# Performance work log

Measured on AMD Instinct MI355X. Metric: run time of the kernel, lower is better.

## Reference

```python
import jax, jax.numpy as jnp
import numpy as np
import math


def setup_inputs() -> dict:
    key = jax.random.key(0)
    kq, kk, kv = jax.random.split(key, 3)
    B, H, N, d = 4, 16, 4096, 128
    return {
        "query": jax.random.normal(kq, (B, H, N, d), dtype=jnp.float32),
        "key": jax.random.normal(kk, (B, H, N, d), dtype=jnp.float32),
        "value": jax.random.normal(kv, (B, H, N, d), dtype=jnp.float32),
        "Br": 128,
        "Bc": 128,
    }


def reference(query, key, value, Br, Bc):
    """Tiled FlashAttention with online softmax (non-MX path of the module).

    Math per inner-loop iteration j (matches _inner_loop_body_sequential):
      scores = Q @ K_j^T * (1/sqrt(d))       (accumulate_fp32=True -> fp32)
      m_new  = max(m, scores.max(-1))
      alpha  = exp(m - m_new)
      P      = exp(scores - m_new)
      l      = alpha*l + P.sum(-1)
      O      = alpha*O + P @ V_j
    Final: out = O / l
    """
    B, H, N, d = query.shape
    Tc = N // Bc
    sm_scale = jnp.float32(1.0 / math.sqrt(d))

    # KV tiles: [Tc, B, H, Bc, d]
    k_tiles = jnp.moveaxis(key.reshape(B, H, Tc, Bc, d), 2, 0)
    v_tiles = jnp.moveaxis(value.reshape(B, H, Tc, Bc, d), 2, 0)

    q = query.astype(jnp.float32)

    O0 = jnp.zeros((B, H, N, d), dtype=jnp.float32)
    l0 = jnp.zeros((B, H, N, 1), dtype=jnp.float32)
    m0 = jnp.full((B, H, N, 1), -jnp.inf, dtype=jnp.float32)

    def body(carry, kv):
        O_i, l_i, m_i = carry
        Kj, Vj = kv  # [B, H, Bc, d]
        s = jnp.einsum("bhqd,bhkd->bhqk", q, Kj.astype(jnp.float32)) * sm_scale
        m_new = jnp.maximum(m_i, jnp.max(s, axis=-1, keepdims=True))
        alpha = jnp.exp(m_i - m_new)
        P = jnp.exp(s - m_new)
        l_new = alpha * l_i + jnp.sum(P, axis=-1, keepdims=True)
        O_new = alpha * O_i + jnp.einsum("bhqk,bhkd->bhqd", P, Vj.astype(jnp.float32))
        return (O_new, l_new, m_new), None

    (O_f, l_f, _), _ = jax.lax.scan(body, (O0, l0, m0), (k_tiles, v_tiles))
    out = O_f / l_f
    return out.astype(query.dtype)
```

## Files before the change

### kernel.cpp

```cpp
#include <hip/hip_runtime.h>
#include <math.h>


#define DHEAD 128
#define SEQ 4096
#define BR 128
#define BC 64
#define TC (SEQ / BC)
#define KSTR 136
#define VSTR 72

#define AS1 __attribute__((address_space(1)))
#define AS3 __attribute__((address_space(3)))

typedef __attribute__((ext_vector_type(8))) short short8;
typedef __attribute__((ext_vector_type(4))) float floatx4;
typedef __attribute__((ext_vector_type(2))) float floatx2;
typedef __attribute__((ext_vector_type(16))) float floatx16;

union U8 { unsigned u[4]; short8 s; };

__device__ __forceinline__ unsigned pk(float a, float b) {
    unsigned ua = __float_as_uint(a) + 0x8000u;
    unsigned ub = __float_as_uint(b) + 0x8000u;
    return __builtin_amdgcn_perm(ub, ua, 0x07060302);
}

__global__ __launch_bounds__(256) void conv_kv(const float* __restrict__ K,
                                               const float* __restrict__ V,
                                               short* __restrict__ Kb,
                                               short* __restrict__ Vb) {
    __shared__ float vt[64 * 133];
    const int blk = blockIdx.x;
    const float* Kh = K + (size_t)blk * (BC * DHEAD);
    const float* Vh = V + (size_t)blk * (BC * DHEAD);
    short* kb = Kb + (size_t)blk * (BC * DHEAD);
    short* vb = Vb + (size_t)blk * (BC * DHEAD);
    const int t = threadIdx.x;

#pragma unroll
    for (int i = 0; i < 4; ++i) {
        int c = i * 256 + t;
        int row = c >> 4;
        int d0 = (((c & 15) ^ ((row & 7) << 1)) << 3);
        const float* s = Kh + row * DHEAD + d0;
        floatx4 f0 = *(const floatx4*)s;
        floatx4 f1 = *(const floatx4*)(s + 4);
        U8 u;
        u.u[0] = pk(f0[0], f0[1]);
        u.u[1] = pk(f0[2], f0[3]);
        u.u[2] = pk(f1[0], f1[1]);
        u.u[3] = pk(f1[2], f1[3]);
        *(short8*)(kb + c * 8) = u.s;
    }

    {
        int n = t >> 2;
        int c0 = (t & 3) * 32;
        const float* s = Vh + n * DHEAD + c0;
        float* d = vt + n * 133 + c0;
#pragma unroll
        for (int j = 0; j < 8; ++j) *(floatx4*)(d + j * 4) = *(const floatx4*)(s + j * 4);
    }
    __syncthreads();

#pragma unroll
    for (int i = 0; i < 4; ++i) {
        int c = i * 256 + t;
        int row = c >> 3;
        int n0 = (((c & 7) ^ (row & 7)) << 3);
        float f[8];
#pragma unroll
        for (int j = 0; j < 8; ++j) f[j] = vt[(n0 + j) * 133 + row];
        U8 u;
        u.u[0] = pk(f[0], f[1]);
        u.u[1] = pk(f[2], f[3]);
        u.u[2] = pk(f[4], f[5]);
        u.u[3] = pk(f[6], f[7]);
        *(short8*)(vb + c * 8) = u.s;
    }
}

__launch_bounds__(256, 3)
__global__ void fa_fwd_ws(const float* __restrict__ Q, const short* __restrict__ Kb,
                          const short* __restrict__ Vb, float* __restrict__ Out) {
    __shared__ __attribute__((aligned(16))) short K_lds[BC * DHEAD];
    __shared__ __attribute__((aligned(16))) short VT_lds[DHEAD * BC];

    int x = blockIdx.x;
    int xcd = x & 7;
    int g = x >> 3;
    int q_tile = g & 31;
    int head = ((g >> 5) << 3) + xcd;

    const float* Qh = Q + (size_t)head * SEQ * DHEAD;
    const short* kbh = Kb + (size_t)head * (SEQ * DHEAD);
    const short* vbh = Vb + (size_t)head * (SEQ * DHEAD);
    float* Oh = Out + (size_t)head * SEQ * DHEAD;

    const int tid = threadIdx.x;
    const int wave = tid >> 6;
    const int lane = tid & 63;
    const int lm = lane & 31;
    const int h = lane >> 5;

    const int q0 = q_tile * BR;
    const int qw = wave * 32;

    const int kx = (lm & 7) << 4;
    const int vx = (lm & 7) << 3;

    const float cscale = 0.12751743f;
    short8 bq[8];
    {
        const float* qrow = Qh + (size_t)(q0 + qw + lm) * DHEAD;
#pragma unroll
        for (int s = 0; s < 8; ++s) {
            floatx4 f0 = *(const floatx4*)(qrow + s * 16 + h * 8);
            floatx4 f1 = *(const floatx4*)(qrow + s * 16 + h * 8 + 4);
            U8 t;
            t.u[0] = pk(f0[0] * cscale, f0[1] * cscale);
            t.u[1] = pk(f0[2] * cscale, f0[3] * cscale);
            t.u[2] = pk(f1[0] * cscale, f1[1] * cscale);
            t.u[3] = pk(f1[2] * cscale, f1[3] * cscale);
            bq[s] = t.s;
        }
    }

    floatx16 oacc[4];
#pragma unroll
    for (int i = 0; i < 4; ++i) oacc[i] = (floatx16)0.0f;
    float l_acc = 0.0f;

    for (int kt = 0; kt < TC; ++kt) {
        __syncthreads();

        {
            const short* kg = kbh + kt * 8192 + wave * 2048 + lane * 8;
            const short* vg = vbh + kt * 8192 + wave * 2048 + lane * 8;
            short* kl = (short*)K_lds + wave * 2048;
            short* vl = (short*)VT_lds + wave * 2048;
#pragma unroll
            for (int i = 0; i < 4; ++i) {
                __builtin_amdgcn_global_load_lds((const AS1 unsigned int*)(kg + i * 512),
                                                 (AS3 unsigned int*)(kl + i * 512), 16, 0, 0);
                __builtin_amdgcn_global_load_lds((const AS1 unsigned int*)(vg + i * 512),
                                                 (AS3 unsigned int*)(vl + i * 512), 16, 0, 0);
            }
        }
        __syncthreads();

        floatx16 sacc[2];
        sacc[0] = (floatx16)0.0f;
        sacc[1] = (floatx16)0.0f;
        __builtin_amdgcn_s_setprio(1);
#pragma unroll
        for (int kc = 0; kc < 8; ++kc) {
#pragma unroll
            for (int nt = 0; nt < 2; ++nt) {
                short8 a = *(const short8*)&K_lds[(nt * 32 + lm) * 128 + ((kc * 16 + h * 8) ^ kx)];
                sacc[nt] = __builtin_amdgcn_mfma_f32_32x32x16_bf16(a, bq[kc], sacc[nt], 0, 0, 0);
            }
        }
        __builtin_amdgcn_s_setprio(0);

#pragma unroll
        for (int nt = 0; nt < 2; ++nt) {
            float e[16];
#pragma unroll
            for (int r = 0; r < 16; ++r) e[r] = exp2f(sacc[nt][r]);
            float t8[8];
#pragma unroll
            for (int i = 0; i < 8; ++i) t8[i] = e[i] + e[8 + i];
            float t4[4];
#pragma unroll
            for (int i = 0; i < 4; ++i) t4[i] = t8[i] + t8[4 + i];
            l_acc += (t4[0] + t4[1]) + (t4[2] + t4[3]);

#pragma unroll
            for (int hf = 0; hf < 2; ++hf) {
                const int b0 = hf * 8;
                unsigned u0 = pk(e[b0 + 0], e[b0 + 1]);
                unsigned u1 = pk(e[b0 + 2], e[b0 + 3]);
                unsigned u2 = pk(e[b0 + 4], e[b0 + 5]);
                unsigned u3 = pk(e[b0 + 6], e[b0 + 7]);
                auto s1 = __builtin_amdgcn_permlane32_swap(u0, u2, false, false);
                auto s2 = __builtin_amdgcn_permlane32_swap(u1, u3, false, false);
                U8 t;
                t.u[0] = s1[0];
                t.u[1] = s2[0];
                t.u[2] = s1[1];
                t.u[3] = s2[1];
                const int kc2 = nt * 2 + hf;
                __builtin_amdgcn_s_setprio(1);
#pragma unroll
                for (int dt = 0; dt < 4; ++dt) {
                    short8 b = *(const short8*)&VT_lds[(dt * 32 + lm) * 64 + ((kc2 * 16 + h * 8) ^ vx)];
                    oacc[dt] = __builtin_amdgcn_mfma_f32_32x32x16_bf16(t.s, b, oacc[dt], 0, 0, 0);
                }
                __builtin_amdgcn_s_setprio(0);
            }
        }
    }

    float l_full = l_acc + __shfl_xor(l_acc, 32);
    float rl[16];
#pragma unroll
    for (int r = 0; r < 16; ++r) {
        int qr = (r & 3) + 8 * (r >> 2) + 4 * h;
        rl[r] = 1.0f / __shfl(l_full, qr);
    }
#pragma unroll
    for (int dt = 0; dt < 4; ++dt)
#pragma unroll
        for (int r = 0; r < 16; ++r) {
            int qr = (r & 3) + 8 * (r >> 2) + 4 * h;
            Oh[(size_t)(q0 + qw + qr) * DHEAD + dt * 32 + lm] = oacc[dt][r] * rl[r];
        }
}

__launch_bounds__(256, 3)
__global__ void fa_fwd(const float* __restrict__ Q, const float* __restrict__ K,
                       const float* __restrict__ V, float* __restrict__ Out) {
    __shared__ __attribute__((aligned(16))) short K_lds[BC * KSTR];
    __shared__ __attribute__((aligned(16))) short VT_lds[DHEAD * VSTR];

    int x = blockIdx.x;
    int xcd = x & 7;
    int g = x >> 3;
    int q_tile = g & 31;
    int head = ((g >> 5) << 3) + xcd;

    const float* Qh = Q + (size_t)head * SEQ * DHEAD;
    const float* Kh = K + (size_t)head * SEQ * DHEAD;
    const float* Vh = V + (size_t)head * SEQ * DHEAD;
    float* Oh = Out + (size_t)head * SEQ * DHEAD;

    const int tid = threadIdx.x;
    const int wave = tid >> 6;
    const int lane = tid & 63;
    const int lm = lane & 31;
    const int h = lane >> 5;

    const int q0 = q_tile * BR;
    const int qw = wave * 32;

    const float cscale = 0.12751743f;
    short8 bq[8];
    {
        const float* qrow = Qh + (size_t)(q0 + qw + lm) * DHEAD;
#pragma unroll
        for (int s = 0; s < 8; ++s) {
            floatx4 f0 = *(const floatx4*)(qrow + s * 16 + h * 8);
            floatx4 f1 = *(const floatx4*)(qrow + s * 16 + h * 8 + 4);
            U8 t;
            t.u[0] = pk(f0[0] * cscale, f0[1] * cscale);
            t.u[1] = pk(f0[2] * cscale, f0[3] * cscale);
            t.u[2] = pk(f1[0] * cscale, f1[1] * cscale);
            t.u[3] = pk(f1[2] * cscale, f1[3] * cscale);
            bq[s] = t.s;
        }
    }

    floatx16 oacc[4];
#pragma unroll
    for (int i = 0; i < 4; ++i) oacc[i] = (floatx16)0.0f;
    float l_acc = 0.0f;

    const int kr = tid & 63;
    const int kc0 = (tid >> 6) * 32;
    const int vd0 = (tid & 63) * 2;
    const int vn0 = (tid >> 6) * 16;

    for (int kt = 0; kt < TC; ++kt) {
        const int kv0 = kt * BC;
        __syncthreads();
        {
            const floatx4* src = (const floatx4*)(Kh + (size_t)(kv0 + kr) * DHEAD + kc0);
            floatx4 f[8];
#pragma unroll
            for (int i = 0; i < 8; ++i) f[i] = src[i];
#pragma unroll
            for (int w = 0; w < 4; ++w) {
                U8 t;
                t.u[0] = pk(f[2 * w][0], f[2 * w][1]);
                t.u[1] = pk(f[2 * w][2], f[2 * w][3]);
                t.u[2] = pk(f[2 * w + 1][0], f[2 * w + 1][1]);
                t.u[3] = pk(f[2 * w + 1][2], f[2 * w + 1][3]);
                *(short8*)&K_lds[kr * KSTR + kc0 + w * 8] = t.s;
            }
        }
        {
            const float* src = Vh + (size_t)(kv0 + vn0) * DHEAD + vd0;
            floatx2 f[16];
#pragma unroll
            for (int j = 0; j < 16; ++j) f[j] = *(const floatx2*)(src + j * DHEAD);
            U8 a0, a1, b0, b1;
#pragma unroll
            for (int p = 0; p < 4; ++p) {
                a0.u[p] = pk(f[2 * p][0], f[2 * p + 1][0]);
                a1.u[p] = pk(f[8 + 2 * p][0], f[9 + 2 * p][0]);
                b0.u[p] = pk(f[2 * p][1], f[2 * p + 1][1]);
                b1.u[p] = pk(f[8 + 2 * p][1], f[9 + 2 * p][1]);
            }
            *(short8*)&VT_lds[vd0 * VSTR + vn0] = a0.s;
            *(short8*)&VT_lds[vd0 * VSTR + vn0 + 8] = a1.s;
            *(short8*)&VT_lds[(vd0 + 1) * VSTR + vn0] = b0.s;
            *(short8*)&VT_lds[(vd0 + 1) * VSTR + vn0 + 8] = b1.s;
        }
        __syncthreads();

        floatx16 sacc[2];
        sacc[0] = (floatx16)0.0f;
        sacc[1] = (floatx16)0.0f;
        __builtin_amdgcn_s_setprio(1);
#pragma unroll
        for (int kc = 0; kc < 8; ++kc) {
#pragma unroll
            for (int nt = 0; nt < 2; ++nt) {
                short8 a = *(const short8*)&K_lds[(nt * 32 + lm) * KSTR + kc * 16 + h * 8];
                sacc[nt] = __builtin_amdgcn_mfma_f32_32x32x16_bf16(a, bq[kc], sacc[nt], 0, 0, 0);
            }
        }
        __builtin_amdgcn_s_setprio(0);

#pragma unroll
        for (int nt = 0; nt < 2; ++nt) {
            float e[16];
#pragma unroll
            for (int r = 0; r < 16; ++r) e[r] = exp2f(sacc[nt][r]);
            float t8[8];
#pragma unroll
            for (int i = 0; i < 8; ++i) t8[i] = e[i] + e[8 + i];
            float t4[4];
#pragma unroll
            for (int i = 0; i < 4; ++i) t4[i] = t8[i] + t8[4 + i];
            l_acc += (t4[0] + t4[1]) + (t4[2] + t4[3]);

#pragma unroll
            for (int hf = 0; hf < 2; ++hf) {
                const int b0 = hf * 8;
                unsigned u0 = pk(e[b0 + 0], e[b0 + 1]);
                unsigned u1 = pk(e[b0 + 2], e[b0 + 3]);
                unsigned u2 = pk(e[b0 + 4], e[b0 + 5]);
                unsigned u3 = pk(e[b0 + 6], e[b0 + 7]);
                auto s1 = __builtin_amdgcn_permlane32_swap(u0, u2, false, false);
                auto s2 = __builtin_amdgcn_permlane32_swap(u1, u3, false, false);
                U8 t;
                t.u[0] = s1[0];
                t.u[1] = s2[0];
                t.u[2] = s1[1];
                t.u[3] = s2[1];
                const int kc2 = nt * 2 + hf;
                __builtin_amdgcn_s_setprio(1);
#pragma unroll
                for (int dt = 0; dt < 4; ++dt) {
                    short8 b = *(const short8*)&VT_lds[(dt * 32 + lm) * VSTR + kc2 * 16 + h * 8];
                    oacc[dt] = __builtin_amdgcn_mfma_f32_32x32x16_bf16(t.s, b, oacc[dt], 0, 0, 0);
                }
                __builtin_amdgcn_s_setprio(0);
            }
        }
    }

    float l_full = l_acc + __shfl_xor(l_acc, 32);
    float rl[16];
#pragma unroll
    for (int r = 0; r < 16; ++r) {
        int qr = (r & 3) + 8 * (r >> 2) + 4 * h;
        rl[r] = 1.0f / __shfl(l_full, qr);
    }
#pragma unroll
    for (int dt = 0; dt < 4; ++dt)
#pragma unroll
        for (int r = 0; r < 16; ++r) {
            int qr = (r & 3) + 8 * (r >> 2) + 4 * h;
            Oh[(size_t)(q0 + qw + qr) * DHEAD + dt * 32 + lm] = oacc[dt][r] * rl[r];
        }
}

extern "C" void kernel_launch(void* const* d_in, const int* in_sizes, int n_in,
                              void* d_out, int out_size, void* d_ws, size_t ws_size,
                              hipStream_t stream) {
    const float* q = (const float*)d_in[0];
    const float* k = (const float*)d_in[1];
    const float* v = (const float*)d_in[2];
    float* out = (float*)d_out;
    const size_t need = (size_t)64 * SEQ * DHEAD * 2 * 2;
    dim3 block(256);
    if (ws_size >= need) {
        short* kb = (short*)d_ws;
        short* vb = kb + (size_t)64 * SEQ * DHEAD;
        hipLaunchKernelGGL(conv_kv, dim3(64 * TC), block, 0, stream, k, v, kb, vb);
        hipLaunchKernelGGL(fa_fwd_ws, dim3(64 * (SEQ / BR)), block, 0, stream, q, kb, vb, out);
    } else {
        hipLaunchKernelGGL(fa_fwd, dim3(64 * (SEQ / BR)), block, 0, stream, q, k, v, out);
    }
}
```

Measured before the change: 962.2 us.

## Double-buffer K tiles and prefetch next K/V via async LDS loads

The attention loop now double-buffers the K tile in LDS and issues the global-to-LDS load for the next K tile before the QK^T MFMAs. The next V tile is loaded right after the PV MFMAs, using vmcnt waits and raw barriers in place of full syncthreads, so memory latency overlaps compute. The K swizzle is changed from a 16-element to an 8-element XOR granularity, and the conversion kernel is split into separate K and V kernels to match. LDS use grows by one extra K tile, which may affect occupancy at 3 blocks per CU.

```diff
diff --git a/kernel.cpp b/kernel.cpp
--- a/kernel.cpp
+++ b/kernel.cpp
@@ -26,23 +26,17 @@
     return __builtin_amdgcn_perm(ub, ua, 0x07060302);
 }
 
-__global__ __launch_bounds__(256) void conv_kv(const float* __restrict__ K,
-                                               const float* __restrict__ V,
-                                               short* __restrict__ Kb,
-                                               short* __restrict__ Vb) {
-    __shared__ float vt[64 * 133];
+__global__ __launch_bounds__(256) void conv_k(const float* __restrict__ K,
+                                              short* __restrict__ Kb) {
     const int blk = blockIdx.x;
     const float* Kh = K + (size_t)blk * (BC * DHEAD);
-    const float* Vh = V + (size_t)blk * (BC * DHEAD);
     short* kb = Kb + (size_t)blk * (BC * DHEAD);
-    short* vb = Vb + (size_t)blk * (BC * DHEAD);
     const int t = threadIdx.x;
-
 #pragma unroll
     for (int i = 0; i < 4; ++i) {
         int c = i * 256 + t;
         int row = c >> 4;
-        int d0 = (((c & 15) ^ ((row & 7) << 1)) << 3);
+        int d0 = (((c & 15) ^ (row & 7)) << 3);
         const float* s = Kh + row * DHEAD + d0;
         floatx4 f0 = *(const floatx4*)s;
         floatx4 f1 = *(const floatx4*)(s + 4);
@@ -53,7 +47,15 @@
         u.u[3] = pk(f1[2], f1[3]);
         *(short8*)(kb + c * 8) = u.s;
     }
-
+}
+
+__global__ __launch_bounds__(256) void conv_v(const float* __restrict__ V,
+                                              short* __restrict__ Vb) {
+    __shared__ float vt[64 * 133];
+    const int blk = blockIdx.x;
+    const float* Vh = V + (size_t)blk * (BC * DHEAD);
+    short* vb = Vb + (size_t)blk * (BC * DHEAD);
+    const int t = threadIdx.x;
     {
         int n = t >> 2;
         int c0 = (t & 3) * 32;
@@ -63,7 +65,6 @@
         for (int j = 0; j < 8; ++j) *(floatx4*)(d + j * 4) = *(const floatx4*)(s + j * 4);
     }
     __syncthreads();
-
 #pragma unroll
     for (int i = 0; i < 4; ++i) {
         int c = i * 256 + t;
@@ -84,7 +85,7 @@
 __launch_bounds__(256, 3)
 __global__ void fa_fwd_ws(const float* __restrict__ Q, const short* __restrict__ Kb,
                           const short* __restrict__ Vb, float* __restrict__ Out) {
-    __shared__ __attribute__((aligned(16))) short K_lds[BC * DHEAD];
+    __shared__ __attribute__((aligned(16))) short K_lds[2 * BC * DHEAD];
     __shared__ __attribute__((aligned(16))) short VT_lds[DHEAD * BC];
 
     int x = blockIdx.x;
@@ -107,7 +108,7 @@
     const int q0 = q_tile * BR;
     const int qw = wave * 32;
 
-    const int kx = (lm & 7) << 4;
+    const int kx = (lm & 7) << 3;
     const int vx = (lm & 7) << 3;
 
     const float cscale = 0.12751743f;
@@ -132,23 +133,39 @@
     for (int i = 0; i < 4; ++i) oacc[i] = (floatx16)0.0f;
     float l_acc = 0.0f;
 
+    const int wlofs = wave * 2048;
+    const int glofs = wave * 2048 + lane * 8;
+
+    {
+        const short* kg = kbh + glofs;
+        const short* vg = vbh + glofs;
+        short* kl = K_lds + wlofs;
+        short* vl = VT_lds + wlofs;
+#pragma unroll
+        for (int i = 0; i < 4; ++i)
+            __builtin_amdgcn_global_load_lds((const AS1 unsigned int*)(kg + i * 512),
+                                             (AS3 unsigned int*)(kl + i * 512), 16, 0, 0);
+#pragma unroll
+        for (int i = 0; i < 4; ++i)
+            __builtin_amdgcn_global_load_lds((const AS1 unsigned int*)(vg + i * 512),
+                                             (AS3 unsigned int*)(vl + i * 512), 16, 0, 0);
+    }
+
+    unsigned kofs_cur = 0, kofs_nxt = 8192;
+
     for (int kt = 0; kt < TC; ++kt) {
-        __syncthreads();
-
-        {
-            const short* kg = kbh + kt * 8192 + wave * 2048 + lane * 8;
-            const short* vg = vbh + kt * 8192 + wave * 2048 + lane * 8;
-            short* kl = (short*)K_lds + wave * 2048;
-            short* vl = (short*)VT_lds + wave * 2048;
-#pragma unroll
-            for (int i = 0; i < 4; ++i) {
+        asm volatile("s_waitcnt vmcnt(4)" ::: "memory");
+        __builtin_amdgcn_s_barrier();
+        __builtin_amdgcn_sched_barrier(0);
+
+        if (kt + 1 < TC) {
+            const short* kg = kbh + (size_t)(kt + 1) * 8192 + glofs;
+            short* kl = K_lds + kofs_nxt + wlofs;
+#pragma unroll
+            for (int i = 0; i < 4; ++i)
                 __builtin_amdgcn_global_load_lds((const AS1 unsigned int*)(kg + i * 512),
                                                  (AS3 unsigned int*)(kl + i * 512), 16, 0, 0);
-                __builtin_amdgcn_global_load_lds((const AS1 unsigned int*)(vg + i * 512),
-                                                 (AS3 unsigned int*)(vl + i * 512), 16, 0, 0);
-            }
-        }
-        __syncthreads();
+        }
 
         floatx16 sacc[2];
         sacc[0] = (floatx16)0.0f;
@@ -158,7 +175,194 @@
         for (int kc = 0; kc < 8; ++kc) {
 #pragma unroll
             for (int nt = 0; nt < 2; ++nt) {
-                short8 a = *(const short8*)&K_lds[(nt * 32 + lm) * 128 + ((kc * 16 + h * 8) ^ kx)];
+                short8 a = *(const short8*)&K_lds[kofs_cur + (nt * 32 + lm) * 128 +
+                                                  ((kc * 16 + h * 8) ^ kx)];
+                sacc[nt] = __builtin_amdgcn_mfma_f32_32x32x16_bf16(a, bq[kc], sacc[nt], 0, 0, 0);
+            }
+        }
+        __builtin_amdgcn_s_setprio(0);
+
+        float e0[16], e1[16];
+#pragma unroll
+        for (int r = 0; r < 16; ++r) e0[r] = exp2f(sacc[0][r]);
+#pragma unroll
+        for (int r = 0; r < 16; ++r) e1[r] = exp2f(sacc[1][r]);
+        {
+            float t8[8];
+#pragma unroll
+            for (int i = 0; i < 8; ++i) t8[i] = (e0[i] + e0[8 + i]) + (e1[i] + e1[8 + i]);
+            float t4[4];
+#pragma unroll
+            for (int i = 0; i < 4; ++i) t4[i] = t8[i] + t8[4 + i];
+            l_acc += (t4[0] + t4[1]) + (t4[2] + t4[3]);
+        }
+        U8 pa[4];
+#pragma unroll
+        for (int nt = 0; nt < 2; ++nt)
+#pragma unroll
+            for (int hf = 0; hf < 2; ++hf) {
+                const float* e = nt ? e1 : e0;
+                const int b0 = hf * 8;
+                unsigned u0 = pk(e[b0 + 0], e[b0 + 1]);
+                unsigned u1 = pk(e[b0 + 2], e[b0 + 3]);
+                unsigned u2 = pk(e[b0 + 4], e[b0 + 5]);
+                unsigned u3 = pk(e[b0 + 6], e[b0 + 7]);
+                auto s1 = __builtin_amdgcn_permlane32_swap(u0, u2, false, false);
+                auto s2 = __builtin_amdgcn_permlane32_swap(u1, u3, false, false);
+                pa[nt * 2 + hf].u[0] = s1[0];
+                pa[nt * 2 + hf].u[1] = s2[0];
+                pa[nt * 2 + hf].u[2] = s1[1];
+                pa[nt * 2 + hf].u[3] = s2[1];
+            }
+
+        if (kt + 1 < TC) {
+            asm volatile("s_waitcnt vmcnt(4)" ::: "memory");
+        } else {
+            asm volatile("s_waitcnt vmcnt(0)" ::: "memory");
+        }
+        __builtin_amdgcn_s_barrier();
+        __builtin_amdgcn_sched_barrier(0);
+
+        __builtin_amdgcn_s_setprio(1);
+#pragma unroll
+        for (int kc2 = 0; kc2 < 4; ++kc2) {
+#pragma unroll
+            for (int dt = 0; dt < 4; ++dt) {
+                short8 b = *(const short8*)&VT_lds[(dt * 32 + lm) * 64 +
+                                                   ((kc2 * 16 + h * 8) ^ vx)];
+                oacc[dt] = __builtin_amdgcn_mfma_f32_32x32x16_bf16(pa[kc2].s, b, oacc[dt], 0, 0, 0);
+            }
+        }
+        __builtin_amdgcn_s_setprio(0);
+
+        if (kt + 1 < TC) {
+            __builtin_amdgcn_s_barrier();
+            const short* vg = vbh + (size_t)(kt + 1) * 8192 + glofs;
+            short* vl = VT_lds + wlofs;
+#pragma unroll
+            for (int i = 0; i < 4; ++i)
+                __builtin_amdgcn_global_load_lds((const AS1 unsigned int*)(vg + i * 512),
+                                                 (AS3 unsigned int*)(vl + i * 512), 16, 0, 0);
+        }
+        unsigned t = kofs_cur; kofs_cur = kofs_nxt; kofs_nxt = t;
+    }
+
+    float l_full = l_acc + __shfl_xor(l_acc, 32);
+    float rl[16];
+#pragma unroll
+    for (int r = 0; r < 16; ++r) {
+        int qr = (r & 3) + 8 * (r >> 2) + 4 * h;
+        rl[r] = 1.0f / __shfl(l_full, qr);
+    }
+#pragma unroll
+    for (int dt = 0; dt < 4; ++dt)
+#pragma unroll
+        for (int r = 0; r < 16; ++r) {
+            int qr = (r & 3) + 8 * (r >> 2) + 4 * h;
+            Oh[(size_t)(q0 + qw + qr) * DHEAD + dt * 32 + lm] = oacc[dt][r] * rl[r];
+        }
+}
+
+__launch_bounds__(256, 3)
+__global__ void fa_fwd(const float* __restrict__ Q, const float* __restrict__ K,
+                       const float* __restrict__ V, float* __restrict__ Out) {
+    __shared__ __attribute__((aligned(16))) short K_lds[BC * KSTR];
+    __shared__ __attribute__((aligned(16))) short VT_lds[DHEAD * VSTR];
+
+    int x = blockIdx.x;
+    int xcd = x & 7;
+    int g = x >> 3;
+    int q_tile = g & 31;
+    int head = ((g >> 5) << 3) + xcd;
+
+    const float* Qh = Q + (size_t)head * SEQ * DHEAD;
+    const float* Kh = K + (size_t)head * SEQ * DHEAD;
+    const float* Vh = V + (size_t)head * SEQ * DHEAD;
+    float* Oh = Out + (size_t)head * SEQ * DHEAD;
+
+    const int tid = threadIdx.x;
+    const int wave = tid >> 6;
+    const int lane = tid & 63;
+    const int lm = lane & 31;
+    const int h = lane >> 5;
+
+    const int q0 = q_tile * BR;
+    const int qw = wave * 32;
+
+    const float cscale = 0.12751743f;
+    short8 bq[8];
+    {
+        const float* qrow = Qh + (size_t)(q0 + qw + lm) * DHEAD;
+#pragma unroll
+        for (int s = 0; s < 8; ++s) {
+            floatx4 f0 = *(const floatx4*)(qrow + s * 16 + h * 8);
+            floatx4 f1 = *(const floatx4*)(qrow + s * 16 + h * 8 + 4);
+            U8 t;
+            t.u[0] = pk(f0[0] * cscale, f0[1] * cscale);
+            t.u[1] = pk(f0[2] * cscale, f0[3] * cscale);
+            t.u[2] = pk(f1[0] * cscale, f1[1] * cscale);
+            t.u[3] = pk(f1[2] * cscale, f1[3] * cscale);
+            bq[s] = t.s;
+        }
+    }
+
+    floatx16 oacc[4];
+#pragma unroll
+    for (int i = 0; i < 4; ++i) oacc[i] = (floatx16)0.0f;
+    float l_acc = 0.0f;
+
+    const int kr = tid & 63;
+    const int kc0 = (tid >> 6) * 32;
+    const int vd0 = (tid & 63) * 2;
+    const int vn0 = (tid >> 6) * 16;
+
+    for (int kt = 0; kt < TC; ++kt) {
+        const int kv0 = kt * BC;
+        __syncthreads();
+        {
+            const floatx4* src = (const floatx4*)(Kh + (size_t)(kv0 + kr) * DHEAD + kc0);
+            floatx4 f[8];
+#pragma unroll
+            for (int i = 0; i < 8; ++i) f[i] = src[i];
+#pragma unroll
+            for (int w = 0; w < 4; ++w) {
+                U8 t;
+                t.u[0] = pk(f[2 * w][0], f[2 * w][1]);
+                t.u[1] = pk(f[2 * w][2], f[2 * w][3]);
+                t.u[2] = pk(f[2 * w + 1][0], f[2 * w + 1][1]);
+                t.u[3] = pk(f[2 * w + 1][2], f[2 * w + 1][3]);
+                *(short8*)&K_lds[kr * KSTR + kc0 + w * 8] = t.s;
+            }
+        }
+        {
+            const float* src = Vh + (size_t)(kv0 + vn0) * DHEAD + vd0;
+            floatx2 f[16];
+#pragma unroll
+            for (int j = 0; j < 16; ++j) f[j] = *(const floatx2*)(src + j * DHEAD);
+            U8 a0, a1, b0, b1;
+#pragma unroll
+            for (int p = 0; p < 4; ++p) {
+                a0.u[p] = pk(f[2 * p][0], f[2 * p + 1][0]);
+                a1.u[p] = pk(f[8 + 2 * p][0], f[9 + 2 * p][0]);
+                b0.u[p] = pk(f[2 * p][1], f[2 * p + 1][1]);
+                b1.u[p] = pk(f[8 + 2 * p][1], f[9 + 2 * p][1]);
+            }
+            *(short8*)&VT_lds[vd0 * VSTR + vn0] = a0.s;
+            *(short8*)&VT_lds[vd0 * VSTR + vn0 + 8] = a1.s;
+            *(short8*)&VT_lds[(vd0 + 1) * VSTR + vn0] = b0.s;
+            *(short8*)&VT_lds[(vd0 + 1) * VSTR + vn0 + 8] = b1.s;
+        }
+        __syncthreads();
+
+        floatx16 sacc[2];
+        sacc[0] = (floatx16)0.0f;
+        sacc[1] = (floatx16)0.0f;
+        __builtin_amdgcn_s_setprio(1);
+#pragma unroll
+        for (int kc = 0; kc < 8; ++kc) {
+#pragma unroll
+            for (int nt = 0; nt < 2; ++nt) {
+                short8 a = *(const short8*)&K_lds[(nt * 32 + lm) * KSTR + kc * 16 + h * 8];
                 sacc[nt] = __builtin_amdgcn_mfma_f32_32x32x16_bf16(a, bq[kc], sacc[nt], 0, 0, 0);
             }
         }
@@ -195,166 +399,6 @@
                 __builtin_amdgcn_s_setprio(1);
 #pragma unroll
                 for (int dt = 0; dt < 4; ++dt) {
-                    short8 b = *(const short8*)&VT_lds[(dt * 32 + lm) * 64 + ((kc2 * 16 + h * 8) ^ vx)];
-                    oacc[dt] = __builtin_amdgcn_mfma_f32_32x32x16_bf16(t.s, b, oacc[dt], 0, 0, 0);
-                }
-                __builtin_amdgcn_s_setprio(0);
-            }
-        }
-    }
-
-    float l_full = l_acc + __shfl_xor(l_acc, 32);
-    float rl[16];
-#pragma unroll
-    for (int r = 0; r < 16; ++r) {
-        int qr = (r & 3) + 8 * (r >> 2) + 4 * h;
-        rl[r] = 1.0f / __shfl(l_full, qr);
-    }
-#pragma unroll
-    for (int dt = 0; dt < 4; ++dt)
-#pragma unroll
-        for (int r = 0; r < 16; ++r) {
-            int qr = (r & 3) + 8 * (r >> 2) + 4 * h;
-            Oh[(size_t)(q0 + qw + qr) * DHEAD + dt * 32 + lm] = oacc[dt][r] * rl[r];
-        }
-}
-
-__launch_bounds__(256, 3)
-__global__ void fa_fwd(const float* __restrict__ Q, const float* __restrict__ K,
-                       const float* __restrict__ V, float* __restrict__ Out) {
-    __shared__ __attribute__((aligned(16))) short K_lds[BC * KSTR];
-    __shared__ __attribute__((aligned(16))) short VT_lds[DHEAD * VSTR];
-
-    int x = blockIdx.x;
-    int xcd = x & 7;
-    int g = x >> 3;
-    int q_tile = g & 31;
-    int head = ((g >> 5) << 3) + xcd;
-
-    const float* Qh = Q + (size_t)head * SEQ * DHEAD;
-    const float* Kh = K + (size_t)head * SEQ * DHEAD;
-    const float* Vh = V + (size_t)head * SEQ * DHEAD;
-    float* Oh = Out + (size_t)head * SEQ * DHEAD;
-
-    const int tid = threadIdx.x;
-    const int wave = tid >> 6;
-    const int lane = tid & 63;
-    const int lm = lane & 31;
-    const int h = lane >> 5;
-
-    const int q0 = q_tile * BR;
-    const int qw = wave * 32;
-
-    const float cscale = 0.12751743f;
-    short8 bq[8];
-    {
-        const float* qrow = Qh + (size_t)(q0 + qw + lm) * DHEAD;
-#pragma unroll
-        for (int s = 0; s < 8; ++s) {
-            floatx4 f0 = *(const floatx4*)(qrow + s * 16 + h * 8);
-            floatx4 f1 = *(const floatx4*)(qrow + s * 16 + h * 8 + 4);
-            U8 t;
-            t.u[0] = pk(f0[0] * cscale, f0[1] * cscale);
-            t.u[1] = pk(f0[2] * cscale, f0[3] * cscale);
-            t.u[2] = pk(f1[0] * cscale, f1[1] * cscale);
-            t.u[3] = pk(f1[2] * cscale, f1[3] * cscale);
-            bq[s] = t.s;
-        }
-    }
-
-    floatx16 oacc[4];
-#pragma unroll
-    for (int i = 0; i < 4; ++i) oacc[i] = (floatx16)0.0f;
-    float l_acc = 0.0f;
-
-    const int kr = tid & 63;
-    const int kc0 = (tid >> 6) * 32;
-    const int vd0 = (tid & 63) * 2;
-    const int vn0 = (tid >> 6) * 16;
-
-    for (int kt = 0; kt < TC; ++kt) {
-        const int kv0 = kt * BC;
-        __syncthreads();
-        {
-            const floatx4* src = (const floatx4*)(Kh + (size_t)(kv0 + kr) * DHEAD + kc0);
-            floatx4 f[8];
-#pragma unroll
-            for (int i = 0; i < 8; ++i) f[i] = src[i];
-#pragma unroll
-            for (int w = 0; w < 4; ++w) {
-                U8 t;
-                t.u[0] = pk(f[2 * w][0], f[2 * w][1]);
-                t.u[1] = pk(f[2 * w][2], f[2 * w][3]);
-                t.u[2] = pk(f[2 * w + 1][0], f[2 * w + 1][1]);
-                t.u[3] = pk(f[2 * w + 1][2], f[2 * w + 1][3]);
-                *(short8*)&K_lds[kr * KSTR + kc0 + w * 8] = t.s;
-            }
-        }
-        {
-            const float* src = Vh + (size_t)(kv0 + vn0) * DHEAD + vd0;
-            floatx2 f[16];
-#pragma unroll
-            for (int j = 0; j < 16; ++j) f[j] = *(const floatx2*)(src + j * DHEAD);
-            U8 a0, a1, b0, b1;
-#pragma unroll
-            for (int p = 0; p < 4; ++p) {
-                a0.u[p] = pk(f[2 * p][0], f[2 * p + 1][0]);
-                a1.u[p] = pk(f[8 + 2 * p][0], f[9 + 2 * p][0]);
-                b0.u[p] = pk(f[2 * p][1], f[2 * p + 1][1]);
-                b1.u[p] = pk(f[8 + 2 * p][1], f[9 + 2 * p][1]);
-            }
-            *(short8*)&VT_lds[vd0 * VSTR + vn0] = a0.s;
-            *(short8*)&VT_lds[vd0 * VSTR + vn0 + 8] = a1.s;
-            *(short8*)&VT_lds[(vd0 + 1) * VSTR + vn0] = b0.s;
-            *(short8*)&VT_lds[(vd0 + 1) * VSTR + vn0 + 8] = b1.s;
-        }
-        __syncthreads();
-
-        floatx16 sacc[2];
-        sacc[0] = (floatx16)0.0f;
-        sacc[1] = (floatx16)0.0f;
-        __builtin_amdgcn_s_setprio(1);
-#pragma unroll
-        for (int kc = 0; kc < 8; ++kc) {
-#pragma unroll
-            for (int nt = 0; nt < 2; ++nt) {
-                short8 a = *(const short8*)&K_lds[(nt * 32 + lm) * KSTR + kc * 16 + h * 8];
-                sacc[nt] = __builtin_amdgcn_mfma_f32_32x32x16_bf16(a, bq[kc], sacc[nt], 0, 0, 0);
-            }
-        }
-        __builtin_amdgcn_s_setprio(0);
-
-#pragma unroll
-        for (int nt = 0; nt < 2; ++nt) {
-            float e[16];
-#pragma unroll
-            for (int r = 0; r < 16; ++r) e[r] = exp2f(sacc[nt][r]);
-            float t8[8];
-#pragma unroll
-            for (int i = 0; i < 8; ++i) t8[i] = e[i] + e[8 + i];
-            float t4[4];
-#pragma unroll
-            for (int i = 0; i < 4; ++i) t4[i] = t8[i] + t8[4 + i];
-            l_acc += (t4[0] + t4[1]) + (t4[2] + t4[3]);
-
-#pragma unroll
-            for (int hf = 0; hf < 2; ++hf) {
-                const int b0 = hf * 8;
-                unsigned u0 = pk(e[b0 + 0], e[b0 + 1]);
-                unsigned u1 = pk(e[b0 + 2], e[b0 + 3]);
-                unsigned u2 = pk(e[b0 + 4], e[b0 + 5]);
-                unsigned u3 = pk(e[b0 + 6], e[b0 + 7]);
-                auto s1 = __builtin_amdgcn_permlane32_swap(u0, u2, false, false);
-                auto s2 = __builtin_amdgcn_permlane32_swap(u1, u3, false, false);
-                U8 t;
-                t.u[0] = s1[0];
-                t.u[1] = s2[0];
-                t.u[2] = s1[1];
-                t.u[3] = s2[1];
-                const int kc2 = nt * 2 + hf;
-                __builtin_amdgcn_s_setprio(1);
-#pragma unroll
-                for (int dt = 0; dt < 4; ++dt) {
                     short8 b = *(const short8*)&VT_lds[(dt * 32 + lm) * VSTR + kc2 * 16 + h * 8];
                     oacc[dt] = __builtin_amdgcn_mfma_f32_32x32x16_bf16(t.s, b, oacc[dt], 0, 0, 0);
                 }
@@ -391,7 +435,8 @@
     if (ws_size >= need) {
         short* kb = (short*)d_ws;
         short* vb = kb + (size_t)64 * SEQ * DHEAD;
-        hipLaunchKernelGGL(conv_kv, dim3(64 * TC), block, 0, stream, k, v, kb, vb);
+        hipLaunchKernelGGL(conv_k, dim3(64 * TC), block, 0, stream, k, kb);
+        hipLaunchKernelGGL(conv_v, dim3(64 * TC), block, 0, stream, v, vb);
         hipLaunchKernelGGL(fa_fwd_ws, dim3(64 * (SEQ / BR)), block, 0, stream, q, kb, vb, out);
     } else {
         hipLaunchKernelGGL(fa_fwd, dim3(64 * (SEQ / BR)), block, 0, stream, q, k, v, out);
```

After: 967.3 us. Within noise of the previous version (+0.5%).
